# Optimization experiments

Hardware: AMD Instinct MI355X
Metric: run time of the kernel (lower is better)

The kernel has to match this reference:

```python
import jax, jax.numpy as jnp
import numpy as np

B, H0, W0, C, NH, G = 2, 256, 256, 64, 4, 8
PD = (C // 4) // 4  # DynamicPosBias pos_dim = 4
HID = 4 * C


def _ln(x, g, b, eps=1e-5):
    mu = jnp.mean(x, -1, keepdims=True)
    var = jnp.mean((x - mu) ** 2, -1, keepdims=True)
    return (x - mu) * jax.lax.rsqrt(var + eps) * g + b


def setup_inputs():
    key = jax.random.key(0)
    ks = iter(jax.random.split(key, 48))
    w = lambda shape: jax.random.normal(next(ks), shape, jnp.float32) * 0.02
    return {
        'x': jax.random.normal(next(ks), (B, H0 * W0, C), jnp.float32),
        'y': jax.random.normal(next(ks), (B, H0 * W0, C), jnp.float32),
        'norm1_g': jnp.ones((C,), jnp.float32), 'norm1_b': jnp.zeros((C,), jnp.float32),
        'qkv_w': w((C, 3 * C)), 'qkv_b': jnp.zeros((3 * C,), jnp.float32),
        'proj_w': w((C, C)), 'proj_b': jnp.zeros((C,), jnp.float32),
        'pp_w': w((2, PD)), 'pp_b': jnp.zeros((PD,), jnp.float32),
        'ln1_g': jnp.ones((PD,), jnp.float32), 'ln1_b': jnp.zeros((PD,), jnp.float32),
        'l1_w': w((PD, PD)), 'l1_b': jnp.zeros((PD,), jnp.float32),
        'ln2_g': jnp.ones((PD,), jnp.float32), 'ln2_b': jnp.zeros((PD,), jnp.float32),
        'l2_w': w((PD, PD)), 'l2_b': jnp.zeros((PD,), jnp.float32),
        'ln3_g': jnp.ones((PD,), jnp.float32), 'ln3_b': jnp.zeros((PD,), jnp.float32),
        'l3_w': w((PD, NH)), 'l3_b': jnp.zeros((NH,), jnp.float32),
        'norm2_g': jnp.ones((C,), jnp.float32), 'norm2_b': jnp.zeros((C,), jnp.float32),
        'fx1_w': w((C, HID)), 'fx1_b': jnp.zeros((HID,), jnp.float32),
        'fx2_w': w((HID, C)), 'fx2_b': jnp.zeros((C,), jnp.float32),
        'fy1_w': w((C, HID)), 'fy1_b': jnp.zeros((HID,), jnp.float32),
        'fy2_w': w((HID, C)), 'fy2_b': jnp.zeros((C,), jnp.float32),
        'H': H0, 'W': W0,
    }


def reference(x, y, norm1_g, norm1_b, qkv_w, qkv_b, proj_w, proj_b,
              pp_w, pp_b, ln1_g, ln1_b, l1_w, l1_b, ln2_g, ln2_b, l2_w, l2_b,
              ln3_g, ln3_b, l3_w, l3_b, norm2_g, norm2_b,
              fx1_w, fx1_b, fx2_w, fx2_b, fy1_w, fy1_b, fy2_w, fy2_b, H, W):
    Bb, L, Cc = x.shape
    d = Cc // NH
    xn = _ln(x, norm1_g, norm1_b).reshape(Bb, H, W, Cc)
    yn = _ln(y, norm1_g, norm1_b).reshape(Bb, H, W, Cc)

    def part(t):  # (B,H,W,C) -> (B*nW, G*G, C)
        t = t.reshape(Bb, H // G, G, W // G, G, Cc).transpose(0, 1, 3, 2, 4, 5)
        return t.reshape(-1, G * G, Cc)

    # merge both modalities' patches of the same window along the token axis
    tok = tok = jnp.concatenate([part(xn), part(yn)], axis=1)  # (B_, 2*G*G, C)
    Gh, Gw = 2 * G, G
    N = Gh * Gw

    # dynamic relative position bias (small MLP + gather)
    bh = jnp.arange(1 - Gh, Gh)
    bw = jnp.arange(1 - Gw, Gw)
    biases = jnp.stack(jnp.meshgrid(bh, bw, indexing='ij'), 0).reshape(2, -1).T.astype(x.dtype)
    coords = jnp.stack(jnp.meshgrid(jnp.arange(Gh), jnp.arange(Gw), indexing='ij'), 0).reshape(2, -1)
    rel = (coords[:, :, None] - coords[:, None, :]).transpose(1, 2, 0)
    ridx = (rel[..., 0] + Gh - 1) * (2 * Gw - 1) + (rel[..., 1] + Gw - 1)  # (N,N)
    p = biases @ pp_w + pp_b
    p = jax.nn.relu(_ln(p, ln1_g, ln1_b)) @ l1_w + l1_b
    p = jax.nn.relu(_ln(p, ln2_g, ln2_b)) @ l2_w + l2_b
    p = jax.nn.relu(_ln(p, ln3_g, ln3_b)) @ l3_w + l3_b  # ((2Gh-1)*(2Gw-1), NH)
    rpb = p[ridx.reshape(-1)].reshape(N, N, NH).transpose(2, 0, 1)  # (NH,N,N)

    # windowed multi-head attention
    qkv = (tok @ qkv_w + qkv_b).reshape(-1, N, 3, NH, d).transpose(2, 0, 3, 1, 4)
    q, k, v = qkv[0] * (d ** -0.5), qkv[1], qkv[2]
    attn = jnp.einsum('bhnd,bhmd->bhnm', q, k) + rpb[None]
    attn = jax.nn.softmax(attn, axis=-1)
    out = jnp.einsum('bhnm,bhmd->bhnd', attn, v).transpose(0, 2, 1, 3).reshape(-1, N, Cc)
    out = out @ proj_w + proj_b

    def rev(t):  # (B*nW, G*G, C) -> (B, H*W, C)
        t = t.reshape(Bb, H // G, W // G, G, G, Cc).transpose(0, 1, 3, 2, 4, 5)
        return t.reshape(Bb, H * W, Cc)

    x = x + rev(out[:, :G * G])
    y = y + rev(out[:, G * G:])

    def mlp(t, w1, b1, w2, b2):
        return jax.nn.gelu(t @ w1 + b1, approximate=False) @ w2 + b2

    x = x + mlp(_ln(x, norm2_g, norm2_b), fx1_w, fx1_b, fx2_w, fx2_b)
    y = y + mlp(_ln(y, norm2_g, norm2_b), fy1_w, fy1_b, fy2_w, fy2_b)
    return x, y
```

## Files before the change

### kernel.cpp

```cpp
#include <hip/hip_runtime.h>
#include <math.h>

constexpr int CC    = 64;
constexpr int GG    = 8;
constexpr int H0    = 256;
constexpr int W0c   = 256;
constexpr int BB    = 2;
constexpr int LL    = H0 * W0c;
constexpr int NWIN  = BB * (H0 / GG) * (W0c / GG);
constexpr int HIDN  = 256;
constexpr int NBIA  = 31 * 15;
constexpr long long MODSZ = (long long)BB * LL * CC;

constexpr float INV_LN2 = 1.4426950408889634f;

constexpr int WS_PTAB  = 0;
constexpr int WS_BIAS  = 8192;
constexpr int WS_WQKV  = 270336;
constexpr int WS_WPROJ = 294912;
constexpr int WS_MLPW  = 303104;

using f32x4  = __attribute__((ext_vector_type(4))) float;
using bf16x8 = __attribute__((ext_vector_type(8))) short;
using bf16x4 = __attribute__((ext_vector_type(4))) short;

static __device__ __forceinline__ short to_bf16(float f) {
  unsigned u = __float_as_uint(f);
  unsigned r = (u + 0x7FFFu + ((u >> 16) & 1u)) >> 16;
  return (short)r;
}
static __device__ __forceinline__ bf16x4 mk4_bf16(float a, float b, float c, float d) {
  unsigned p0 = ((__float_as_uint(a) + 0x8000u) >> 16) | ((__float_as_uint(b) + 0x8000u) & 0xFFFF0000u);
  unsigned p1 = ((__float_as_uint(c) + 0x8000u) >> 16) | ((__float_as_uint(d) + 0x8000u) & 0xFFFF0000u);
  bf16x4 r;
  r[0] = (short)(p0 & 0xFFFFu); r[1] = (short)(p0 >> 16);
  r[2] = (short)(p1 & 0xFFFFu); r[3] = (short)(p1 >> 16);
  return r;
}
static __device__ __forceinline__ float gelu_tanh(float u) {
  float u2 = u * u;
  float t  = fmaf(0.044715f, u2, 1.0f);
  float z  = u * t * 1.5957691216057308f;
  float e  = __expf(-z);
  return u / (1.0f + e);
}

static __device__ __forceinline__ void ln4_relu(float* p, const float* g, const float* b) {
  float mu = 0.25f * (p[0] + p[1] + p[2] + p[3]);
  float d0 = p[0] - mu, d1 = p[1] - mu, d2 = p[2] - mu, d3 = p[3] - mu;
  float var = 0.25f * (d0 * d0 + d1 * d1 + d2 * d2 + d3 * d3);
  float rs = rsqrtf(var + 1e-5f);
  p[0] = fmaxf(d0 * rs * g[0] + b[0], 0.0f);
  p[1] = fmaxf(d1 * rs * g[1] + b[1], 0.0f);
  p[2] = fmaxf(d2 * rs * g[2] + b[2], 0.0f);
  p[3] = fmaxf(d3 * rs * g[3] + b[3], 0.0f);
}
static __device__ __forceinline__ void mm4(const float* a, const float* w, const float* b, float* o) {
  #pragma unroll
  for (int j = 0; j < 4; ++j) {
    float s = b[j];
    #pragma unroll
    for (int i = 0; i < 4; ++i) s += a[i] * w[i * 4 + j];
    o[j] = s;
  }
}

__global__ void pbias_kernel(const float* __restrict__ pp_w, const float* __restrict__ pp_b,
                             const float* __restrict__ ln1g, const float* __restrict__ ln1b,
                             const float* __restrict__ l1w,  const float* __restrict__ l1b,
                             const float* __restrict__ ln2g, const float* __restrict__ ln2b,
                             const float* __restrict__ l2w,  const float* __restrict__ l2b,
                             const float* __restrict__ ln3g, const float* __restrict__ ln3b,
                             const float* __restrict__ l3w,  const float* __restrict__ l3b,
                             float* __restrict__ p_table) {
  int r = blockIdx.x * blockDim.x + threadIdx.x;
  if (r >= NBIA) return;
  float bh = (float)(r / 15 - 15);
  float bw = (float)(r % 15 - 7);
  float a[4], t[4];
  #pragma unroll
  for (int j = 0; j < 4; ++j) a[j] = bh * pp_w[j] + bw * pp_w[4 + j] + pp_b[j];
  ln4_relu(a, ln1g, ln1b);
  mm4(a, l1w, l1b, t);
  ln4_relu(t, ln2g, ln2b);
  mm4(t, l2w, l2b, a);
  ln4_relu(a, ln3g, ln3b);
  mm4(a, l3w, l3b, t);
  #pragma unroll
  for (int j = 0; j < 4; ++j) p_table[r * 4 + j] = t[j];
}

__global__ void bias_expand_kernel(const float* __restrict__ p_table, float* __restrict__ bias_exp) {
  int gid = blockIdx.x * 256 + threadIdx.x;
  int h   = gid >> 12;
  int rem = gid & 4095;
  int q   = rem >> 5;
  int k0  = (rem & 31) * 4;
  int qih = q >> 3, qiw = q & 7;
  float o[4];
  #pragma unroll
  for (int kk = 0; kk < 4; ++kk) {
    int k = k0 + kk;
    int ridx = (qih - (k >> 3) + 15) * 15 + (qiw - (k & 7) + 7);
    o[kk] = p_table[ridx * 4 + h] * INV_LN2;
  }
  f32x4 v = {o[0], o[1], o[2], o[3]};
  *(f32x4*)(bias_exp + gid * 4) = v;
}

__global__ void prep_w_kernel(const float* __restrict__ qkv_w, const float* __restrict__ proj_w,
                              short* __restrict__ wqkvF, short* __restrict__ projF) {
  int t = blockIdx.x * 256 + threadIdx.x;
  if (t < 12288) {
    int slot = t >> 9, e = t & 511;
    int lp = e >> 3, j = e & 7;
    int ng = slot >> 1, s = slot & 1;
    int k   = 32 * s + 8 * (lp >> 4) + j;
    int col = 16 * ng + (lp & 15);
    float v = qkv_w[k * 192 + col];
    if (col < 64) v *= 0.25f * INV_LN2;
    wqkvF[t] = to_bf16(v);
  } else {
    int t2 = t - 12288;
    int slot = t2 >> 9, e = t2 & 511;
    int lp = e >> 3, j = e & 7;
    int ng = slot >> 1, s = slot & 1;
    int k   = 32 * s + 8 * (lp >> 4) + j;
    int col = 16 * ng + (lp & 15);
    projF[t2] = to_bf16(proj_w[k * 64 + col]);
  }
}

__global__ void prep_mlp_w_kernel(const float* __restrict__ fx1w, const float* __restrict__ fy1w,
                                  const float* __restrict__ fx2w, const float* __restrict__ fy2w,
                                  short* __restrict__ mlpW) {
  int gid = blockIdx.x * 256 + threadIdx.x;
  int img = gid >> 14;
  int e   = gid & 16383;
  int slot = e >> 9, lp = (e >> 3) & 63, j = e & 7;
  float v;
  if (img < 2) {
    const float* w1 = img ? fy1w : fx1w;
    int nt = slot >> 1, ks = slot & 1;
    int in_ch = ks * 32 + ((lp >> 4) << 3) + j;
    int hid   = nt * 16 + (lp & 15);
    v = w1[in_ch * HIDN + hid];
  } else {
    const float* w2 = (img & 1) ? fy2w : fx2w;
    int nt2 = slot >> 3, g2 = slot & 7;
    int hid = g2 * 32 + ((lp >> 4) << 3) + j;
    int oc  = nt2 * 16 + (lp & 15);
    v = w2[hid * CC + oc];
  }
  mlpW[gid] = to_bf16(v);
}


#define ATT_LOADB(biasreg, qt) { \
  _Pragma("unroll") \
  for (int kt_ = 0; kt_ < 8; ++kt_) \
    biasreg[kt_] = *(const f32x4*)(biasH + (16 * (qt) + l15) * 128 + 16 * kt_ + 4 * lg); }

#define ATT_LOADQ(qfreg, qt) { \
  qfreg = (bf16x8){0, 0, 0, 0, 0, 0, 0, 0}; \
  if (l < 32) { \
    int row_ = 16 * (qt) + l15; \
    qfreg = *(const bf16x8*)(QB_ + ((row_ * 128 + h * 32 + lg * 16) ^ ((row_ & 7) << 4))); } }

#define ATT_BODY(qt, biasreg, qfreg) { \
  f32x4 s_[8]; \
  _Pragma("unroll") \
  for (int kt_ = 0; kt_ < 8; ++kt_) \
    s_[kt_] = __builtin_amdgcn_mfma_f32_16x16x32_bf16(kf[kt_], qfreg, biasreg[kt_], 0, 0, 0); \
  float sum_ = 0.0f; \
  _Pragma("unroll") \
  for (int kt_ = 0; kt_ < 8; ++kt_) { \
    s_[kt_][0] = __builtin_amdgcn_exp2f(s_[kt_][0]); \
    s_[kt_][1] = __builtin_amdgcn_exp2f(s_[kt_][1]); \
    s_[kt_][2] = __builtin_amdgcn_exp2f(s_[kt_][2]); \
    s_[kt_][3] = __builtin_amdgcn_exp2f(s_[kt_][3]); \
    sum_ += (s_[kt_][0] + s_[kt_][1]) + (s_[kt_][2] + s_[kt_][3]); } \
  sum_ += __shfl_xor(sum_, 16); \
  sum_ += __shfl_xor(sum_, 32); \
  float inv_ = 1.0f / sum_; \
  _Pragma("unroll") \
  for (int kt_ = 0; kt_ < 8; ++kt_) { \
    int k0_ = 16 * kt_ + 4 * lg; \
    *(bf16x4*)(PBw + ((l15 * 256 + k0_ * 2) ^ pswz)) = mk4_bf16(s_[kt_][0], s_[kt_][1], s_[kt_][2], s_[kt_][3]); } \
  f32x4 pacc_ = {0.0f, 0.0f, 0.0f, 0.0f}; \
  _Pragma("unroll") \
  for (int ks_ = 0; ks_ < 4; ++ks_) { \
    bf16x8 pa_ = *(const bf16x8*)(PBw + ((l15 * 256 + ks_ * 64 + lg * 16) ^ pswz)); \
    pacc_ = __builtin_amdgcn_mfma_f32_16x16x32_bf16(vf[ks_], pa_, pacc_, 0, 0, 0); } \
  pacc_[0] *= inv_; pacc_[1] *= inv_; pacc_[2] *= inv_; pacc_[3] *= inv_; \
  *(bf16x4*)(TOK_ + (((16 * (qt) + l15) * 128 + (h * 16 + lg * 4) * 2) ^ (((16 * (qt) + l15) & 7) << 4))) \
      = mk4_bf16(pacc_[0], pacc_[1], pacc_[2], pacc_[3]); }

__launch_bounds__(256, 2)
__global__ void win_attn_kernel(const float* __restrict__ x, const float* __restrict__ y,
                                const float* __restrict__ n1g, const float* __restrict__ n1b,
                                const float* __restrict__ qkv_b, const float* __restrict__ proj_b,
                                const float* __restrict__ bias_exp,
                                const short* __restrict__ wqkvF, const short* __restrict__ projF,
                                float* __restrict__ out) {
  __shared__ __align__(16) char smem[81920];
  char* const TOK_ = smem;
  char* const QB_  = smem + 16384;
  char* const KB_  = smem + 32768;
  char* const VT_  = smem + 49152;
  char* const PB_  = smem + 65536;

  const int tid = threadIdx.x;
  const int l   = tid & 63;
  const int l15 = l & 15;
  const int lg  = l >> 4;
  const int wv  = __builtin_amdgcn_readfirstlane(tid >> 6);

  const int widx = blockIdx.x;
  const int b  = widx >> 10;
  const int wl = widx & 1023;
  const int wh = wl >> 5, ww = wl & 31;

  {
    const int lane16 = tid & 15;
    const float4 g4 = *(const float4*)(n1g + lane16 * 4);
    const float4 b4 = *(const float4*)(n1b + lane16 * 4);
    #pragma unroll
    for (int ps = 0; ps < 8; ++ps) {
      int t  = ps * 16 + (tid >> 4);
      int g  = t & 63;
      const float* src = ((t & 64) ? y : x)
          + ((long long)b * LL + (long long)(wh * GG + (g >> 3)) * W0c + (ww * GG + (g & 7))) * CC
          + lane16 * 4;
      float4 v = *(const float4*)src;
      float s  = v.x + v.y + v.z + v.w;
      float s2 = v.x * v.x + v.y * v.y + v.z * v.z + v.w * v.w;
      #pragma unroll
      for (int m = 1; m < 16; m <<= 1) { s += __shfl_xor(s, m); s2 += __shfl_xor(s2, m); }
      float mu  = s * (1.0f / 64.0f);
      float var = fmaxf(s2 * (1.0f / 64.0f) - mu * mu, 0.0f);
      float rs  = rsqrtf(var + 1e-5f);
      bf16x4 w4 = mk4_bf16((v.x - mu) * rs * g4.x + b4.x,
                           (v.y - mu) * rs * g4.y + b4.y,
                           (v.z - mu) * rs * g4.z + b4.z,
                           (v.w - mu) * rs * g4.w + b4.w);
      *(bf16x4*)(TOK_ + ((t * 128 + lane16 * 8) ^ ((t & 7) << 4))) = w4;
    }
  }
  __syncthreads();

  {
    bf16x8 awq[2][2];
    #pragma unroll
    for (int ct = 0; ct < 2; ++ct)
      #pragma unroll
      for (int ks = 0; ks < 2; ++ks)
        awq[ct][ks] = *(const bf16x8*)((const char*)wqkvF + ((((2 * wv + ct) * 2 + ks)) << 10) + l * 16);
    bf16x8 bwv[2];
    #pragma unroll
    for (int ks = 0; ks < 2; ++ks)
      bwv[ks] = *(const bf16x8*)((const char*)wqkvF + (((8 + wv) * 2 + ks) << 10) + l * 16);

    f32x4 bq[2];
    #pragma unroll
    for (int ct = 0; ct < 2; ++ct) {
      f32x4 bb = *(const f32x4*)(qkv_b + (2 * wv + ct) * 16 + lg * 4);
      if (wv < 2) {
        const float qs = 0.25f * INV_LN2;
        bb[0] *= qs; bb[1] *= qs; bb[2] *= qs; bb[3] *= qs;
      }
      bq[ct] = bb;
    }
    const float bv = qkv_b[128 + wv * 16 + l15];
    char* const QKbuf = (wv < 2) ? QB_ : KB_;
    const int chv = wv * 16 + l15;
    const int vswz = (chv & 7) << 4;

    #pragma unroll
    for (int nt = 0; nt < 8; ++nt) {
      const int row = 16 * nt + l15;
      const int rswz = (row & 7) << 4;
      bf16x8 t0 = *(const bf16x8*)(TOK_ + ((row * 128 +  0 + lg * 16) ^ rswz));
      bf16x8 t1 = *(const bf16x8*)(TOK_ + ((row * 128 + 64 + lg * 16) ^ rswz));
      #pragma unroll
      for (int ct = 0; ct < 2; ++ct) {
        f32x4 a = bq[ct];
        a = __builtin_amdgcn_mfma_f32_16x16x32_bf16(awq[ct][0], t0, a, 0, 0, 0);
        a = __builtin_amdgcn_mfma_f32_16x16x32_bf16(awq[ct][1], t1, a, 0, 0, 0);
        int chL = (((2 * wv + ct) * 16) & 63) + lg * 4;
        *(bf16x4*)(QKbuf + ((row * 128 + chL * 2) ^ rswz)) = mk4_bf16(a[0], a[1], a[2], a[3]);
      }
      {
        f32x4 a = {bv, bv, bv, bv};
        a = __builtin_amdgcn_mfma_f32_16x16x32_bf16(t0, bwv[0], a, 0, 0, 0);
        a = __builtin_amdgcn_mfma_f32_16x16x32_bf16(t1, bwv[1], a, 0, 0, 0);
        int tok0 = 16 * nt + lg * 4;
        *(bf16x4*)(VT_ + ((chv * 256 + tok0 * 2) ^ vswz)) = mk4_bf16(a[0], a[1], a[2], a[3]);
      }
    }
  }
  __syncthreads();

  {
    const int h = wv;
    const float* biasH = bias_exp + h * 16384;
    bf16x8 kf[8];
    #pragma unroll
    for (int kt = 0; kt < 8; ++kt) {
      bf16x8 f = {0, 0, 0, 0, 0, 0, 0, 0};
      if (l < 32) {
        int row = 16 * kt + l15;
        f = *(const bf16x8*)(KB_ + ((row * 128 + h * 32 + lg * 16) ^ ((row & 7) << 4)));
      }
      kf[kt] = f;
    }
    bf16x8 vf[4];
    #pragma unroll
    for (int ks = 0; ks < 4; ++ks) {
      int row = h * 16 + l15;
      vf[ks] = *(const bf16x8*)(VT_ + ((row * 256 + ks * 64 + lg * 16) ^ ((row & 7) << 4)));
    }
    char* const PBw = PB_ + wv * 4096;
    const int pswz = (l15 & 7) << 4;

    f32x4 biasE[8], biasO[8];
    bf16x8 qfE, qfO;
    ATT_LOADB(biasE, 0);
    ATT_LOADQ(qfE, 0);
    #pragma unroll
    for (int qq = 0; qq < 4; ++qq) {
      ATT_LOADB(biasO, 2 * qq + 1);
      ATT_LOADQ(qfO, 2 * qq + 1);
      ATT_BODY(2 * qq, biasE, qfE);
      if (qq < 3) {
        ATT_LOADB(biasE, 2 * qq + 2);
        ATT_LOADQ(qfE, 2 * qq + 2);
      }
      ATT_BODY(2 * qq + 1, biasO, qfO);
    }
  }
  __syncthreads();

  {
    bf16x8 pa2[2];
    #pragma unroll
    for (int ks = 0; ks < 2; ++ks)
      pa2[ks] = *(const bf16x8*)((const char*)projF + (((wv * 2 + ks)) << 10) + l * 16);
    const f32x4 bp = *(const f32x4*)(proj_b + wv * 16 + lg * 4);
    #pragma unroll
    for (int nt = 0; nt < 8; ++nt) {
      const int row = 16 * nt + l15;
      const int rswz = (row & 7) << 4;
      bf16x8 t0 = *(const bf16x8*)(TOK_ + ((row * 128 +  0 + lg * 16) ^ rswz));
      bf16x8 t1 = *(const bf16x8*)(TOK_ + ((row * 128 + 64 + lg * 16) ^ rswz));
      f32x4 acc = bp;
      acc = __builtin_amdgcn_mfma_f32_16x16x32_bf16(pa2[0], t0, acc, 0, 0, 0);
      acc = __builtin_amdgcn_mfma_f32_16x16x32_bf16(pa2[1], t1, acc, 0, 0, 0);
      int g = row & 63;
      long long base = ((long long)b * LL + (long long)(wh * GG + (g >> 3)) * W0c + (ww * GG + (g & 7))) * CC
                       + wv * 16 + lg * 4;
      const float* src = ((row & 64) ? y : x) + base;
      float* dst = out + ((row & 64) ? MODSZ : 0) + base;
      f32x4 sv = *(const f32x4*)src;
      sv[0] += acc[0]; sv[1] += acc[1]; sv[2] += acc[2]; sv[3] += acc[3];
      *(f32x4*)dst = sv;
    }
  }
}

__launch_bounds__(256, 3)
__global__ void mlp_mfma_kernel(const float* __restrict__ n2g, const float* __restrict__ n2b,
                                const float* __restrict__ fx1b, const float* __restrict__ fx2b,
                                const float* __restrict__ fy1b, const float* __restrict__ fy2b,
                                const short* __restrict__ mlpW, float* __restrict__ out) {
  __shared__ __align__(16) char AR4[4][8192];

  const int tid = threadIdx.x;
  const int l   = tid & 63;
  const int l15 = l & 15;
  const int lg  = l >> 4;
  const int wv  = tid >> 6;
  const int bid = blockIdx.x;
  const int mod = bid >> 10;
  const long long wtok0 = (long long)(bid & 1023) * 128 + wv * 32;

  const float* b1 = mod ? fy1b : fx1b;
  const float* b2 = mod ? fy2b : fx2b;
  const short* w1T = mlpW + mod * 16384;
  const short* w2T = mlpW + 32768 + mod * 16384;
  float* const outm = out + (long long)mod * MODSZ;

  char* const TOKw = AR4[wv];
  char* const HBw  = AR4[wv] + 4608;

  {
    const f32x4 g4 = *(const f32x4*)(n2g + l15 * 4);
    const f32x4 b4 = *(const f32x4*)(n2b + l15 * 4);
    #pragma unroll
    for (int ps = 0; ps < 8; ++ps) {
      int t = ps * 4 + lg;
      const float* rp = outm + (wtok0 + t) * CC + l15 * 4;
      f32x4 v = *(const f32x4*)rp;
      float s  = v[0] + v[1] + v[2] + v[3];
      float s2 = v[0] * v[0] + v[1] * v[1] + v[2] * v[2] + v[3] * v[3];
      #pragma unroll
      for (int m = 1; m < 16; m <<= 1) { s += __shfl_xor(s, m); s2 += __shfl_xor(s2, m); }
      float mu  = s * (1.0f / 64.0f);
      float var = fmaxf(s2 * (1.0f / 64.0f) - mu * mu, 0.0f);
      float rs  = rsqrtf(var + 1e-5f);
      bf16x4 w4 = mk4_bf16((v[0] - mu) * rs * g4[0] + b4[0],
                           (v[1] - mu) * rs * g4[1] + b4[1],
                           (v[2] - mu) * rs * g4[2] + b4[2],
                           (v[3] - mu) * rs * g4[3] + b4[3]);
      *(bf16x4*)(TOKw + t * 144 + l15 * 8) = w4;
    }
  }

  bf16x8 tokB[2][2];
  #pragma unroll
  for (int ct = 0; ct < 2; ++ct)
    #pragma unroll
    for (int ks = 0; ks < 2; ++ks)
      tokB[ct][ks] = *(const bf16x8*)(TOKw + (16 * ct + l15) * 144 + ks * 64 + lg * 16);

  f32x4 acc2[4][2];
  #pragma unroll
  for (int n = 0; n < 4; ++n) {
    f32x4 bb = *(const f32x4*)(b2 + n * 16 + lg * 4);
    acc2[n][0] = bb; acc2[n][1] = bb;
  }

  #pragma unroll 1
  for (int g2 = 0; g2 < 8; ++g2) {
    #pragma unroll
    for (int sub = 0; sub < 2; ++sub) {
      const int nt = g2 * 2 + sub;
      bf16x8 wa0 = *(const bf16x8*)(w1T + ((nt * 2 + 0) << 9) + l * 8);
      bf16x8 wa1 = *(const bf16x8*)(w1T + ((nt * 2 + 1) << 9) + l * 8);
      f32x4 z = {0.0f, 0.0f, 0.0f, 0.0f};
      f32x4 d0 = __builtin_amdgcn_mfma_f32_16x16x32_bf16(wa0, tokB[0][0], z, 0, 0, 0);
      d0 = __builtin_amdgcn_mfma_f32_16x16x32_bf16(wa1, tokB[0][1], d0, 0, 0, 0);
      f32x4 d1 = __builtin_amdgcn_mfma_f32_16x16x32_bf16(wa0, tokB[1][0], z, 0, 0, 0);
      d1 = __builtin_amdgcn_mfma_f32_16x16x32_bf16(wa1, tokB[1][1], d1, 0, 0, 0);
      f32x4 b1v = *(const f32x4*)(b1 + nt * 16 + lg * 4);
      bf16x4 h0 = mk4_bf16(gelu_tanh(d0[0] + b1v[0]), gelu_tanh(d0[1] + b1v[1]),
                           gelu_tanh(d0[2] + b1v[2]), gelu_tanh(d0[3] + b1v[3]));
      bf16x4 h1 = mk4_bf16(gelu_tanh(d1[0] + b1v[0]), gelu_tanh(d1[1] + b1v[1]),
                           gelu_tanh(d1[2] + b1v[2]), gelu_tanh(d1[3] + b1v[3]));
      *(bf16x4*)(HBw + l15 * 80        + sub * 32 + lg * 8) = h0;
      *(bf16x4*)(HBw + (16 + l15) * 80 + sub * 32 + lg * 8) = h1;
    }
    bf16x8 hb0 = *(const bf16x8*)(HBw + l15 * 80        + lg * 16);
    bf16x8 hb1 = *(const bf16x8*)(HBw + (16 + l15) * 80 + lg * 16);
    #pragma unroll
    for (int n = 0; n < 4; ++n) {
      bf16x8 wa = *(const bf16x8*)(w2T + ((n * 8 + g2) << 9) + l * 8);
      acc2[n][0] = __builtin_amdgcn_mfma_f32_16x16x32_bf16(wa, hb0, acc2[n][0], 0, 0, 0);
      acc2[n][1] = __builtin_amdgcn_mfma_f32_16x16x32_bf16(wa, hb1, acc2[n][1], 0, 0, 0);
    }
  }

  #pragma unroll
  for (int n = 0; n < 4; ++n)
    #pragma unroll
    for (int ct = 0; ct < 2; ++ct) {
      float* rp = outm + (wtok0 + 16 * ct + l15) * CC + n * 16 + lg * 4;
      f32x4 o = *(const f32x4*)rp;
      o[0] += acc2[n][ct][0]; o[1] += acc2[n][ct][1];
      o[2] += acc2[n][ct][2]; o[3] += acc2[n][ct][3];
      *(f32x4*)rp = o;
    }
}

extern "C" void kernel_launch(void* const* d_in, const int* in_sizes, int n_in,
                              void* d_out, int out_size, void* d_ws, size_t ws_size,
                              hipStream_t stream) {
  const float* x      = (const float*)d_in[0];
  const float* y      = (const float*)d_in[1];
  const float* n1g    = (const float*)d_in[2];
  const float* n1b    = (const float*)d_in[3];
  const float* qkv_w  = (const float*)d_in[4];
  const float* qkv_b  = (const float*)d_in[5];
  const float* proj_w = (const float*)d_in[6];
  const float* proj_b = (const float*)d_in[7];
  const float* pp_w   = (const float*)d_in[8];
  const float* pp_b   = (const float*)d_in[9];
  const float* ln1g   = (const float*)d_in[10];
  const float* ln1b   = (const float*)d_in[11];
  const float* l1w    = (const float*)d_in[12];
  const float* l1b    = (const float*)d_in[13];
  const float* ln2g   = (const float*)d_in[14];
  const float* ln2b   = (const float*)d_in[15];
  const float* l2w    = (const float*)d_in[16];
  const float* l2b    = (const float*)d_in[17];
  const float* ln3g   = (const float*)d_in[18];
  const float* ln3b   = (const float*)d_in[19];
  const float* l3w    = (const float*)d_in[20];
  const float* l3b    = (const float*)d_in[21];
  const float* n2g    = (const float*)d_in[22];
  const float* n2b    = (const float*)d_in[23];
  const float* fx1w   = (const float*)d_in[24];
  const float* fx1b   = (const float*)d_in[25];
  const float* fx2w   = (const float*)d_in[26];
  const float* fx2b   = (const float*)d_in[27];
  const float* fy1w   = (const float*)d_in[28];
  const float* fy1b   = (const float*)d_in[29];
  const float* fy2w   = (const float*)d_in[30];
  const float* fy2b   = (const float*)d_in[31];
  (void)in_sizes; (void)n_in; (void)out_size; (void)ws_size;

  float* out = (float*)d_out;
  char*  ws  = (char*)d_ws;
  float* p_table  = (float*)(ws + WS_PTAB);
  float* bias_exp = (float*)(ws + WS_BIAS);
  short* wqkvF    = (short*)(ws + WS_WQKV);
  short* projF    = (short*)(ws + WS_WPROJ);
  short* mlpW     = (short*)(ws + WS_MLPW);

  pbias_kernel<<<1, 512, 0, stream>>>(pp_w, pp_b, ln1g, ln1b, l1w, l1b,
                                      ln2g, ln2b, l2w, l2b, ln3g, ln3b, l3w, l3b, p_table);
  bias_expand_kernel<<<64, 256, 0, stream>>>(p_table, bias_exp);
  prep_w_kernel<<<64, 256, 0, stream>>>(qkv_w, proj_w, wqkvF, projF);
  prep_mlp_w_kernel<<<256, 256, 0, stream>>>(fx1w, fy1w, fx2w, fy2w, mlpW);
  win_attn_kernel<<<NWIN, 256, 0, stream>>>(x, y, n1g, n1b, qkv_b, proj_b,
                                            bias_exp, wqkvF, projF, out);
  mlp_mfma_kernel<<<2048, 256, 0, stream>>>(n2g, n2b, fx1b, fx2b, fy1b, fy2b,
                                            mlpW, out);
}
```

Baseline: 169.0 us.

## Fuse window attention and MLP into one kernel keeping residual in LDS

Merges the attention kernel and the MLP kernel into a single kernel. The post-attention residual for each window's 128 tokens stays in shared memory, so the MLP reads it from there instead of from global memory. Waves 0-1 handle the x tokens and waves 2-3 the y tokens. This drops one full global write plus read of the intermediate and one kernel launch. In exchange, the MLP runs at the attention kernel's occupancy (2 blocks per CU) instead of 3 and adds a block-wide barrier.

```diff
diff --git a/kernel.cpp b/kernel.cpp
--- a/kernel.cpp
+++ b/kernel.cpp
@@ -197,18 +197,24 @@
       = mk4_bf16(pacc_[0], pacc_[1], pacc_[2], pacc_[3]); }
 
 __launch_bounds__(256, 2)
-__global__ void win_attn_kernel(const float* __restrict__ x, const float* __restrict__ y,
-                                const float* __restrict__ n1g, const float* __restrict__ n1b,
-                                const float* __restrict__ qkv_b, const float* __restrict__ proj_b,
-                                const float* __restrict__ bias_exp,
-                                const short* __restrict__ wqkvF, const short* __restrict__ projF,
-                                float* __restrict__ out) {
+__global__ void fused_kernel(const float* __restrict__ x, const float* __restrict__ y,
+                             const float* __restrict__ n1g, const float* __restrict__ n1b,
+                             const float* __restrict__ qkv_b, const float* __restrict__ proj_b,
+                             const float* __restrict__ bias_exp,
+                             const short* __restrict__ wqkvF, const short* __restrict__ projF,
+                             const float* __restrict__ n2g, const float* __restrict__ n2b,
+                             const float* __restrict__ fx1b, const float* __restrict__ fx2b,
+                             const float* __restrict__ fy1b, const float* __restrict__ fy2b,
+                             const short* __restrict__ mlpW,
+                             float* __restrict__ out) {
   __shared__ __align__(16) char smem[81920];
-  char* const TOK_ = smem;
-  char* const QB_  = smem + 16384;
-  char* const KB_  = smem + 32768;
-  char* const VT_  = smem + 49152;
-  char* const PB_  = smem + 65536;
+  char* const TOK_  = smem;
+  char* const QB_   = smem + 16384;
+  char* const KB_   = smem + 32768;
+  char* const VT_   = smem + 49152;
+  char* const PB_   = smem + 65536;
+  char* const TOKF_ = smem + 16384;
+  char* const MAR_  = smem + 49152;
 
   const int tid = threadIdx.x;
   const int l   = tid & 63;
@@ -360,116 +366,104 @@
       long long base = ((long long)b * LL + (long long)(wh * GG + (g >> 3)) * W0c + (ww * GG + (g & 7))) * CC
                        + wv * 16 + lg * 4;
       const float* src = ((row & 64) ? y : x) + base;
-      float* dst = out + ((row & 64) ? MODSZ : 0) + base;
       f32x4 sv = *(const f32x4*)src;
       sv[0] += acc[0]; sv[1] += acc[1]; sv[2] += acc[2]; sv[3] += acc[3];
-      *(f32x4*)dst = sv;
-    }
-  }
-}
-
-__launch_bounds__(256, 3)
-__global__ void mlp_mfma_kernel(const float* __restrict__ n2g, const float* __restrict__ n2b,
-                                const float* __restrict__ fx1b, const float* __restrict__ fx2b,
-                                const float* __restrict__ fy1b, const float* __restrict__ fy2b,
-                                const short* __restrict__ mlpW, float* __restrict__ out) {
-  __shared__ __align__(16) char AR4[4][8192];
-
-  const int tid = threadIdx.x;
-  const int l   = tid & 63;
-  const int l15 = l & 15;
-  const int lg  = l >> 4;
-  const int wv  = tid >> 6;
-  const int bid = blockIdx.x;
-  const int mod = bid >> 10;
-  const long long wtok0 = (long long)(bid & 1023) * 128 + wv * 32;
-
-  const float* b1 = mod ? fy1b : fx1b;
-  const float* b2 = mod ? fy2b : fx2b;
-  const short* w1T = mlpW + mod * 16384;
-  const short* w2T = mlpW + 32768 + mod * 16384;
-  float* const outm = out + (long long)mod * MODSZ;
-
-  char* const TOKw = AR4[wv];
-  char* const HBw  = AR4[wv] + 4608;
+      *(f32x4*)(TOKF_ + row * 256 + (((wv * 64 + lg * 16)) ^ rswz)) = sv;
+    }
+  }
+  __syncthreads();
 
   {
-    const f32x4 g4 = *(const f32x4*)(n2g + l15 * 4);
-    const f32x4 b4 = *(const f32x4*)(n2b + l15 * 4);
-    #pragma unroll
-    for (int ps = 0; ps < 8; ++ps) {
-      int t = ps * 4 + lg;
-      const float* rp = outm + (wtok0 + t) * CC + l15 * 4;
-      f32x4 v = *(const f32x4*)rp;
-      float s  = v[0] + v[1] + v[2] + v[3];
-      float s2 = v[0] * v[0] + v[1] * v[1] + v[2] * v[2] + v[3] * v[3];
-      #pragma unroll
-      for (int m = 1; m < 16; m <<= 1) { s += __shfl_xor(s, m); s2 += __shfl_xor(s2, m); }
-      float mu  = s * (1.0f / 64.0f);
-      float var = fmaxf(s2 * (1.0f / 64.0f) - mu * mu, 0.0f);
-      float rs  = rsqrtf(var + 1e-5f);
-      bf16x4 w4 = mk4_bf16((v[0] - mu) * rs * g4[0] + b4[0],
-                           (v[1] - mu) * rs * g4[1] + b4[1],
-                           (v[2] - mu) * rs * g4[2] + b4[2],
-                           (v[3] - mu) * rs * g4[3] + b4[3]);
-      *(bf16x4*)(TOKw + t * 144 + l15 * 8) = w4;
-    }
-  }
-
-  bf16x8 tokB[2][2];
-  #pragma unroll
-  for (int ct = 0; ct < 2; ++ct)
-    #pragma unroll
-    for (int ks = 0; ks < 2; ++ks)
-      tokB[ct][ks] = *(const bf16x8*)(TOKw + (16 * ct + l15) * 144 + ks * 64 + lg * 16);
-
-  f32x4 acc2[4][2];
-  #pragma unroll
-  for (int n = 0; n < 4; ++n) {
-    f32x4 bb = *(const f32x4*)(b2 + n * 16 + lg * 4);
-    acc2[n][0] = bb; acc2[n][1] = bb;
-  }
-
-  #pragma unroll 1
-  for (int g2 = 0; g2 < 8; ++g2) {
-    #pragma unroll
-    for (int sub = 0; sub < 2; ++sub) {
-      const int nt = g2 * 2 + sub;
-      bf16x8 wa0 = *(const bf16x8*)(w1T + ((nt * 2 + 0) << 9) + l * 8);
-      bf16x8 wa1 = *(const bf16x8*)(w1T + ((nt * 2 + 1) << 9) + l * 8);
-      f32x4 z = {0.0f, 0.0f, 0.0f, 0.0f};
-      f32x4 d0 = __builtin_amdgcn_mfma_f32_16x16x32_bf16(wa0, tokB[0][0], z, 0, 0, 0);
-      d0 = __builtin_amdgcn_mfma_f32_16x16x32_bf16(wa1, tokB[0][1], d0, 0, 0, 0);
-      f32x4 d1 = __builtin_amdgcn_mfma_f32_16x16x32_bf16(wa0, tokB[1][0], z, 0, 0, 0);
-      d1 = __builtin_amdgcn_mfma_f32_16x16x32_bf16(wa1, tokB[1][1], d1, 0, 0, 0);
-      f32x4 b1v = *(const f32x4*)(b1 + nt * 16 + lg * 4);
-      bf16x4 h0 = mk4_bf16(gelu_tanh(d0[0] + b1v[0]), gelu_tanh(d0[1] + b1v[1]),
-                           gelu_tanh(d0[2] + b1v[2]), gelu_tanh(d0[3] + b1v[3]));
-      bf16x4 h1 = mk4_bf16(gelu_tanh(d1[0] + b1v[0]), gelu_tanh(d1[1] + b1v[1]),
-                           gelu_tanh(d1[2] + b1v[2]), gelu_tanh(d1[3] + b1v[3]));
-      *(bf16x4*)(HBw + l15 * 80        + sub * 32 + lg * 8) = h0;
-      *(bf16x4*)(HBw + (16 + l15) * 80 + sub * 32 + lg * 8) = h1;
-    }
-    bf16x8 hb0 = *(const bf16x8*)(HBw + l15 * 80        + lg * 16);
-    bf16x8 hb1 = *(const bf16x8*)(HBw + (16 + l15) * 80 + lg * 16);
+    const int mod = wv >> 1;
+    const float* b1 = mod ? fy1b : fx1b;
+    const float* b2 = mod ? fy2b : fx2b;
+    const short* w1T = mlpW + mod * 16384;
+    const short* w2T = mlpW + 32768 + mod * 16384;
+    char* const TOKw = MAR_ + wv * 8192;
+    char* const HBw  = TOKw + 4608;
+
+    {
+      const f32x4 g4 = *(const f32x4*)(n2g + l15 * 4);
+      const f32x4 b4 = *(const f32x4*)(n2b + l15 * 4);
+      #pragma unroll
+      for (int ps = 0; ps < 8; ++ps) {
+        int t   = ps * 4 + lg;
+        int row = wv * 32 + t;
+        f32x4 v = *(const f32x4*)(TOKF_ + row * 256 + ((l15 * 16) ^ ((row & 7) << 4)));
+        float s  = v[0] + v[1] + v[2] + v[3];
+        float s2 = v[0] * v[0] + v[1] * v[1] + v[2] * v[2] + v[3] * v[3];
+        #pragma unroll
+        for (int m = 1; m < 16; m <<= 1) { s += __shfl_xor(s, m); s2 += __shfl_xor(s2, m); }
+        float mu  = s * (1.0f / 64.0f);
+        float var = fmaxf(s2 * (1.0f / 64.0f) - mu * mu, 0.0f);
+        float rs  = rsqrtf(var + 1e-5f);
+        bf16x4 w4 = mk4_bf16((v[0] - mu) * rs * g4[0] + b4[0],
+                             (v[1] - mu) * rs * g4[1] + b4[1],
+                             (v[2] - mu) * rs * g4[2] + b4[2],
+                             (v[3] - mu) * rs * g4[3] + b4[3]);
+        *(bf16x4*)(TOKw + t * 144 + l15 * 8) = w4;
+      }
+    }
+
+    bf16x8 tokB[2][2];
+    #pragma unroll
+    for (int ct = 0; ct < 2; ++ct)
+      #pragma unroll
+      for (int ks = 0; ks < 2; ++ks)
+        tokB[ct][ks] = *(const bf16x8*)(TOKw + (16 * ct + l15) * 144 + ks * 64 + lg * 16);
+
+    f32x4 acc2[4][2];
     #pragma unroll
     for (int n = 0; n < 4; ++n) {
-      bf16x8 wa = *(const bf16x8*)(w2T + ((n * 8 + g2) << 9) + l * 8);
-      acc2[n][0] = __builtin_amdgcn_mfma_f32_16x16x32_bf16(wa, hb0, acc2[n][0], 0, 0, 0);
-      acc2[n][1] = __builtin_amdgcn_mfma_f32_16x16x32_bf16(wa, hb1, acc2[n][1], 0, 0, 0);
-    }
-  }
-
-  #pragma unroll
-  for (int n = 0; n < 4; ++n)
-    #pragma unroll
-    for (int ct = 0; ct < 2; ++ct) {
-      float* rp = outm + (wtok0 + 16 * ct + l15) * CC + n * 16 + lg * 4;
-      f32x4 o = *(const f32x4*)rp;
-      o[0] += acc2[n][ct][0]; o[1] += acc2[n][ct][1];
-      o[2] += acc2[n][ct][2]; o[3] += acc2[n][ct][3];
-      *(f32x4*)rp = o;
-    }
+      f32x4 bb = *(const f32x4*)(b2 + n * 16 + lg * 4);
+      acc2[n][0] = bb; acc2[n][1] = bb;
+    }
+
+    #pragma unroll 1
+    for (int g2 = 0; g2 < 8; ++g2) {
+      #pragma unroll
+      for (int sub = 0; sub < 2; ++sub) {
+        const int nt = g2 * 2 + sub;
+        bf16x8 wa0 = *(const bf16x8*)(w1T + ((nt * 2 + 0) << 9) + l * 8);
+        bf16x8 wa1 = *(const bf16x8*)(w1T + ((nt * 2 + 1) << 9) + l * 8);
+        f32x4 z = {0.0f, 0.0f, 0.0f, 0.0f};
+        f32x4 d0 = __builtin_amdgcn_mfma_f32_16x16x32_bf16(wa0, tokB[0][0], z, 0, 0, 0);
+        d0 = __builtin_amdgcn_mfma_f32_16x16x32_bf16(wa1, tokB[0][1], d0, 0, 0, 0);
+        f32x4 d1 = __builtin_amdgcn_mfma_f32_16x16x32_bf16(wa0, tokB[1][0], z, 0, 0, 0);
+        d1 = __builtin_amdgcn_mfma_f32_16x16x32_bf16(wa1, tokB[1][1], d1, 0, 0, 0);
+        f32x4 b1v = *(const f32x4*)(b1 + nt * 16 + lg * 4);
+        bf16x4 h0 = mk4_bf16(gelu_tanh(d0[0] + b1v[0]), gelu_tanh(d0[1] + b1v[1]),
+                             gelu_tanh(d0[2] + b1v[2]), gelu_tanh(d0[3] + b1v[3]));
+        bf16x4 h1 = mk4_bf16(gelu_tanh(d1[0] + b1v[0]), gelu_tanh(d1[1] + b1v[1]),
+                             gelu_tanh(d1[2] + b1v[2]), gelu_tanh(d1[3] + b1v[3]));
+        *(bf16x4*)(HBw + l15 * 80        + sub * 32 + lg * 8) = h0;
+        *(bf16x4*)(HBw + (16 + l15) * 80 + sub * 32 + lg * 8) = h1;
+      }
+      bf16x8 hb0 = *(const bf16x8*)(HBw + l15 * 80        + lg * 16);
+      bf16x8 hb1 = *(const bf16x8*)(HBw + (16 + l15) * 80 + lg * 16);
+      #pragma unroll
+      for (int n = 0; n < 4; ++n) {
+        bf16x8 wa = *(const bf16x8*)(w2T + ((n * 8 + g2) << 9) + l * 8);
+        acc2[n][0] = __builtin_amdgcn_mfma_f32_16x16x32_bf16(wa, hb0, acc2[n][0], 0, 0, 0);
+        acc2[n][1] = __builtin_amdgcn_mfma_f32_16x16x32_bf16(wa, hb1, acc2[n][1], 0, 0, 0);
+      }
+    }
+
+    #pragma unroll
+    for (int n = 0; n < 4; ++n)
+      #pragma unroll
+      for (int ct = 0; ct < 2; ++ct) {
+        int row = wv * 32 + 16 * ct + l15;
+        int ch  = n * 16 + lg * 4;
+        f32x4 r = *(const f32x4*)(TOKF_ + row * 256 + ((ch * 4) ^ ((row & 7) << 4)));
+        r[0] += acc2[n][ct][0]; r[1] += acc2[n][ct][1];
+        r[2] += acc2[n][ct][2]; r[3] += acc2[n][ct][3];
+        int g = row & 63;
+        long long base = ((long long)b * LL + (long long)(wh * GG + (g >> 3)) * W0c + (ww * GG + (g & 7))) * CC + ch;
+        float* dst = out + ((row & 64) ? MODSZ : 0) + base;
+        *(f32x4*)dst = r;
+      }
+  }
 }
 
 extern "C" void kernel_launch(void* const* d_in, const int* in_sizes, int n_in,
@@ -522,8 +516,7 @@
   bias_expand_kernel<<<64, 256, 0, stream>>>(p_table, bias_exp);
   prep_w_kernel<<<64, 256, 0, stream>>>(qkv_w, proj_w, wqkvF, projF);
   prep_mlp_w_kernel<<<256, 256, 0, stream>>>(fx1w, fy1w, fx2w, fy2w, mlpW);
-  win_attn_kernel<<<NWIN, 256, 0, stream>>>(x, y, n1g, n1b, qkv_b, proj_b,
-                                            bias_exp, wqkvF, projF, out);
-  mlp_mfma_kernel<<<2048, 256, 0, stream>>>(n2g, n2b, fx1b, fx2b, fy1b, fy2b,
-                                            mlpW, out);
-}
+  fused_kernel<<<NWIN, 256, 0, stream>>>(x, y, n1g, n1b, qkv_b, proj_b,
+                                         bias_exp, wqkvF, projF,
+                                         n2g, n2b, fx1b, fx2b, fy1b, fy2b, mlpW, out);
+}
```

After: 155.4 us. 8.1% less time.
